# Kernel tuning notes

Measured on AMD Instinct MI355X. Metric: run time of the kernel, lower is better.

Reference implementation:

```python
import jax, jax.numpy as jnp
import numpy as np

B, S, H = 32, 1024, 768          # batch, seq_len, bert hidden
E, W, P = 128, 8, 512            # entities/sample, span width, rel pairs/sample
NT, NR = 5, 9                    # entity types, relation types
D1, HEADS1, D2, RD = 128, 2, 64, 32
REL_IN = 2 * D2 + RD + H         # 928


def _layernorm(x, g, b):
    m = x.mean(-1, keepdims=True)
    v = x.var(-1, keepdims=True)
    return (x - m) * jax.lax.rsqrt(v + 1e-5) * g + b


def _gat_dense(x, Wm, a_src, a_dst, bias, concat):
    # Fully-connected entity graph (incl. self-loops, PyG GATConv default).
    Bn, En, _ = x.shape
    Hh, D = a_src.shape
    h = (x @ Wm).reshape(Bn, En, Hh, D)                      # [B,E,h,D]
    s = jnp.einsum('behd,hd->beh', h, a_src)                 # source score
    d = jnp.einsum('behd,hd->beh', h, a_dst)                 # target score
    # edge j->i : e_ij = leaky_relu(s_j + d_i)
    e = jax.nn.leaky_relu(d[:, :, None, :] + s[:, None, :, :], 0.2)  # [B,i,j,h]
    alpha = jax.nn.softmax(e, axis=2)
    o = jnp.einsum('bijh,bjhd->bihd', alpha, h)
    o = o.reshape(Bn, En, Hh * D) if concat else o.mean(axis=2)
    return o + bias


def setup_inputs() -> dict:
    key = jax.random.key(0)
    ks = jax.random.split(key, 20)
    f = lambda k, shape: jax.random.normal(k, shape, jnp.float32) * 0.02
    return dict(
        sequence_output=jax.random.normal(ks[0], (B, S, H), jnp.float32),
        entity_starts=jax.random.randint(ks[1], (B, E), 0, S - W),
        entity_type_ids=jax.random.randint(ks[2], (B, E), 0, NT),
        pair_idx=jax.random.randint(ks[3], (B, P, 2), 0, E),
        rel_type_ids=jax.random.randint(ks[4], (B, P), 0, NR),
        entity_type_emb=f(ks[5], (NT, H)),
        rel_type_emb=f(ks[6], (NR, RD)),
        W1=f(ks[7], (H, HEADS1 * D1)), a_src1=f(ks[8], (HEADS1, D1)),
        a_dst1=f(ks[9], (HEADS1, D1)), b1=jnp.zeros((HEADS1 * D1,), jnp.float32),
        ln1_g=jnp.ones((HEADS1 * D1,), jnp.float32), ln1_b=jnp.zeros((HEADS1 * D1,), jnp.float32),
        W2=f(ks[10], (HEADS1 * D1, D2)), a_src2=f(ks[11], (1, D2)),
        a_dst2=f(ks[12], (1, D2)), b2=jnp.zeros((D2,), jnp.float32),
        ln2_g=jnp.ones((D2,), jnp.float32), ln2_b=jnp.zeros((D2,), jnp.float32),
        Wr1=f(ks[13], (REL_IN, 256)), br1=jnp.zeros((256,), jnp.float32),
        Wr2=f(ks[14], (256, 1)), br2=jnp.zeros((1,), jnp.float32),
    )


def reference(sequence_output, entity_starts, entity_type_ids, pair_idx, rel_type_ids,
              entity_type_emb, rel_type_emb,
              W1, a_src1, a_dst1, b1, ln1_g, ln1_b,
              W2, a_src2, a_dst2, b2, ln2_g, ln2_b,
              Wr1, br1, Wr2, br2):
    bidx = jnp.arange(B)[:, None]
    # --- per-entity attention pooling over span tokens ---
    tok_idx = entity_starts[:, :, None] + jnp.arange(W)            # [B,E,W]
    toks = sequence_output[jnp.arange(B)[:, None, None], tok_idx]  # [B,E,W,H]
    mean = toks.mean(axis=2)                                       # [B,E,H]
    attn = jax.nn.softmax(jnp.einsum('bewh,beh->bew', toks, mean), axis=-1)
    pooled = jnp.einsum('bew,bewh->beh', attn, toks)
    x = pooled + entity_type_emb[entity_type_ids]                  # [B,E,H]
    # --- 2-layer GAT over fully-connected entity graph ---
    x = jax.nn.elu(_layernorm(_gat_dense(x, W1, a_src1, a_dst1, b1, True), ln1_g, ln1_b))
    x = jax.nn.elu(_layernorm(_gat_dense(x, W2, a_src2, a_dst2, b2, False), ln2_g, ln2_b))
    # --- gather-concat relation MLP scoring ---
    cls = sequence_output[:, 0, :]                                 # [B,H]
    x1 = x[bidx, pair_idx[:, :, 0]]                                # [B,P,64]
    x2 = x[bidx, pair_idx[:, :, 1]]
    rel = rel_type_emb[rel_type_ids]                               # [B,P,32]
    pv = jnp.concatenate([x1, x2, rel, jnp.broadcast_to(cls[:, None, :], (B, P, H))], axis=-1)
    scores = (jax.nn.relu(pv @ Wr1 + br1) @ Wr2 + br2)[..., 0]     # [B,P]
    return scores
```

## Files before the change

### kernel.cpp

```cpp
#include <hip/hip_runtime.h>
#include <hip/hip_bf16.h>

#define BB 32
#define SS 1024
#define HHH 768
#define EE 128
#define WW 8
#define PP 512
#define RDD 32

typedef __attribute__((ext_vector_type(8))) short bf16x8;
typedef __attribute__((ext_vector_type(8))) unsigned short us8;
typedef __attribute__((ext_vector_type(4))) unsigned short us4;
typedef __attribute__((ext_vector_type(4))) float f32x4;

__device__ __forceinline__ unsigned short f2bf(float v) {
    __hip_bfloat16 h = __float2bfloat16(v);
    return *(unsigned short*)&h;
}
__device__ __forceinline__ float bf2f(unsigned short u) {
    unsigned int x = ((unsigned int)u) << 16;
    float f; __builtin_memcpy(&f, &x, 4);
    return f;
}

__global__ __launch_bounds__(256) void pool_prep_kernel(
    const float* __restrict__ seq, const int* __restrict__ starts,
    const int* __restrict__ types, const float* __restrict__ temb,
    unsigned short* __restrict__ xout,
    const float* __restrict__ W1, unsigned short* __restrict__ Wt,
    const float* __restrict__ Wr1, unsigned short* __restrict__ Wtr,
    const float* __restrict__ W2, unsigned short* __restrict__ W2t,
    const float* __restrict__ remb, unsigned short* __restrict__ rembb,
    float* __restrict__ basep) {
    int tid = threadIdx.x;
    __shared__ float sbuf[WW * HHH];
    __shared__ float scred[WW];
    __shared__ float attn_s[WW];

    if (blockIdx.x < BB * EE) {
        int be = blockIdx.x;
        int b = be >> 7;
        int start = starts[be];
        const float4* bp4 = (const float4*)(seq + ((size_t)b * SS + start) * HHH);
        for (int idx = tid; idx < WW * (HHH / 4); idx += 256) {
            int w = idx / (HHH / 4), h4 = idx % (HHH / 4);
            float4 v = bp4[(size_t)w * (HHH / 4) + h4];
            sbuf[w * HHH + h4 * 4 + 0] = v.x; sbuf[w * HHH + h4 * 4 + 1] = v.y;
            sbuf[w * HHH + h4 * 4 + 2] = v.z; sbuf[w * HHH + h4 * 4 + 3] = v.w;
        }
        __syncthreads();

        float sc[WW];
#pragma unroll
        for (int w = 0; w < WW; w++) sc[w] = 0.f;
#pragma unroll
        for (int c = 0; c < 3; c++) {
            int h = tid + 256 * c;
            float s = 0.f;
#pragma unroll
            for (int w = 0; w < WW; w++) s += sbuf[w * HHH + h];
            float m = s * (1.0f / WW);
#pragma unroll
            for (int w = 0; w < WW; w++) sc[w] += sbuf[w * HHH + h] * m;
        }
        if (tid < WW) scred[tid] = 0.f;
        __syncthreads();
        int lane = tid & 63;
#pragma unroll
        for (int w = 0; w < WW; w++) {
            float v = sc[w];
            for (int o = 32; o > 0; o >>= 1) v += __shfl_down(v, o, 64);
            if (lane == 0) atomicAdd(&scred[w], v);
        }
        __syncthreads();
        if (tid == 0) {
            float mx = scred[0];
            for (int w = 1; w < WW; w++) mx = fmaxf(mx, scred[w]);
            float ssum = 0.f;
            float a[WW];
            for (int w = 0; w < WW; w++) { a[w] = __expf(scred[w] - mx); ssum += a[w]; }
            float inv = 1.f / ssum;
            for (int w = 0; w < WW; w++) attn_s[w] = a[w] * inv;
        }
        __syncthreads();

        int t = types[be];
        const float* emb = temb + (size_t)t * HHH;
#pragma unroll
        for (int c = 0; c < 3; c++) {
            int h = tid + 256 * c;
            float p = 0.f;
#pragma unroll
            for (int w = 0; w < WW; w++) p += attn_s[w] * sbuf[w * HHH + h];
            xout[(size_t)be * HHH + h] = f2bf(p + emb[h]);
        }
        return;
    }

    int blk = blockIdx.x - BB * EE;
    if (blk < 48) {
        int k0 = blk * 16;
        for (int i = tid; i < 16 * 256; i += 256)
            sbuf[i] = W1[(size_t)(k0 + (i >> 8)) * 256 + (i & 255)];
        __syncthreads();
        int n = tid;
        us8 v0, v1;
#pragma unroll
        for (int kk = 0; kk < 8; kk++) v0[kk] = f2bf(sbuf[kk * 256 + n]);
#pragma unroll
        for (int kk = 0; kk < 8; kk++) v1[kk] = f2bf(sbuf[(8 + kk) * 256 + n]);
        *(us8*)(Wt + (size_t)n * HHH + k0) = v0;
        *(us8*)(Wt + (size_t)n * HHH + k0 + 8) = v1;
    } else if (blk < 58) {
        int k0 = (blk - 48) * 16;
        for (int i = tid; i < 16 * 256; i += 256)
            sbuf[i] = Wr1[(size_t)(k0 + (i >> 8)) * 256 + (i & 255)];
        __syncthreads();
        int n = tid;
        us8 v0, v1;
#pragma unroll
        for (int kk = 0; kk < 8; kk++) v0[kk] = f2bf(sbuf[kk * 256 + n]);
#pragma unroll
        for (int kk = 0; kk < 8; kk++) v1[kk] = f2bf(sbuf[(8 + kk) * 256 + n]);
        *(us8*)(Wtr + (size_t)n * 160 + k0) = v0;
        *(us8*)(Wtr + (size_t)n * 160 + k0 + 8) = v1;
    } else if (blk < 74) {
        int k0 = (blk - 58) * 16;
        for (int i = tid; i < 16 * 64; i += 256)
            sbuf[(i >> 6) * 64 + (i & 63)] = W2[(size_t)(k0 + (i >> 6)) * 64 + (i & 63)];
        __syncthreads();
        if (tid < 64) {
            int n = tid;
            us8 v0, v1;
#pragma unroll
            for (int kk = 0; kk < 8; kk++) v0[kk] = f2bf(sbuf[kk * 64 + n]);
#pragma unroll
            for (int kk = 0; kk < 8; kk++) v1[kk] = f2bf(sbuf[(8 + kk) * 64 + n]);
            *(us8*)(W2t + (size_t)n * 256 + k0) = v0;
            *(us8*)(W2t + (size_t)n * 256 + k0 + 8) = v1;
        }
    } else if (blk == 74) {
        for (int i = tid; i < 9 * RDD; i += 256) rembb[i] = f2bf(remb[i]);
    } else {
        int pc = blk - 75;
        int kc = pc % 12;
        int b = pc / 12;
        int n = tid;
        if (n < 64) sbuf[4096 + n] = seq[(size_t)b * SS * HHH + kc * 64 + n];
        __syncthreads();
        float acc = 0.f;
        const float* w = Wr1 + (size_t)(160 + kc * 64) * 256 + n;
#pragma unroll 16
        for (int k = 0; k < 64; k++) acc += sbuf[4096 + k] * w[(size_t)k * 256];
        basep[((size_t)kc * 32 + b) * 256 + n] = acc;
    }
}

__global__ __launch_bounds__(256) void gemm1_mfma_kernel(
    const unsigned short* __restrict__ Xb, const unsigned short* __restrict__ Wt,
    float* __restrict__ C) {
    const int K = HHH;
    int n0 = blockIdx.x * 64;
    int m0 = blockIdx.y * 64;
    int tid = threadIdx.x;
    int wave = tid >> 6, lane = tid & 63;
    int wm = (wave >> 1) * 32, wn = (wave & 1) * 32;

    __shared__ __align__(16) unsigned short As[64][40];
    __shared__ __align__(16) unsigned short Bs[64][40];

    f32x4 acc[2][2] = {};
    int ar = tid >> 2;
    int ac = (tid & 3) * 8;
    int fr = lane & 15;
    int fk = (lane >> 4) * 8;

    for (int k0 = 0; k0 < K; k0 += 32) {
        us8 av = *(const us8*)(Xb + (size_t)(m0 + ar) * K + k0 + ac);
        us8 bv = *(const us8*)(Wt + (size_t)(n0 + ar) * K + k0 + ac);
        *(us8*)(&As[ar][ac]) = av;
        *(us8*)(&Bs[ar][ac]) = bv;
        __syncthreads();

        bf16x8 a0 = *(const bf16x8*)(&As[wm + fr][fk]);
        bf16x8 a1 = *(const bf16x8*)(&As[wm + 16 + fr][fk]);
        bf16x8 b0 = *(const bf16x8*)(&Bs[wn + fr][fk]);
        bf16x8 b1 = *(const bf16x8*)(&Bs[wn + 16 + fr][fk]);

        acc[0][0] = __builtin_amdgcn_mfma_f32_16x16x32_bf16(a0, b0, acc[0][0], 0, 0, 0);
        acc[0][1] = __builtin_amdgcn_mfma_f32_16x16x32_bf16(a0, b1, acc[0][1], 0, 0, 0);
        acc[1][0] = __builtin_amdgcn_mfma_f32_16x16x32_bf16(a1, b0, acc[1][0], 0, 0, 0);
        acc[1][1] = __builtin_amdgcn_mfma_f32_16x16x32_bf16(a1, b1, acc[1][1], 0, 0, 0);
        __syncthreads();
    }

    int crow = (lane >> 4) * 4;
    int ccol = lane & 15;
#pragma unroll
    for (int mi = 0; mi < 2; mi++)
#pragma unroll
        for (int ni = 0; ni < 2; ni++)
#pragma unroll
            for (int r = 0; r < 4; r++)
                C[(size_t)(m0 + wm + mi * 16 + crow + r) * 256 +
                  n0 + wn + ni * 16 + ccol] = acc[mi][ni][r];
}

__global__ __launch_bounds__(256) void gat1_fused_kernel(
    const float* __restrict__ h1, const float* __restrict__ a_src1,
    const float* __restrict__ a_dst1, const float* __restrict__ b1,
    const float* __restrict__ gamma, const float* __restrict__ beta,
    unsigned short* __restrict__ g1b) {
    int b = blockIdx.x;
    int tid = threadIdx.x;
    int wave = tid >> 6, lane = tid & 63;
    int wm = wave * 32;
    int fr = lane & 15;
    int fk = (lane >> 4) * 8;

    __shared__ __align__(16) unsigned short h1T[2][128][136];
    __shared__ float ssh[2][128];
    __shared__ float dsh[2][128];

    {
        const float4* src4 = (const float4*)(h1 + (size_t)b * 128 * 256);
        for (int it = 0; it < 32; it++) {
            int i4 = tid + it * 256;
            int j = i4 >> 6;
            int c4 = i4 & 63;
            float4 v = src4[(size_t)j * 64 + c4];
            int d = c4 * 4;
            int hh = d >> 7, dl = d & 127;
            h1T[hh][dl + 0][j] = f2bf(v.x);
            h1T[hh][dl + 1][j] = f2bf(v.y);
            h1T[hh][dl + 2][j] = f2bf(v.z);
            h1T[hh][dl + 3][j] = f2bf(v.w);
        }
    }
    __syncthreads();

    {
        int hh = tid >> 7, j = tid & 127;
        const float* as = a_src1 + hh * 128;
        const float* ad = a_dst1 + hh * 128;
        float s_ = 0.f, d_ = 0.f;
        for (int d2 = 0; d2 < 128; d2++) {
            float hv = bf2f(h1T[hh][d2][j]);
            s_ += hv * as[d2];
            d_ += hv * ad[d2];
        }
        ssh[hh][j] = s_;
        dsh[hh][j] = d_;
    }
    __syncthreads();

    bf16x8 afrag[2][2][4];
#pragma unroll
    for (int hh = 0; hh < 2; hh++)
#pragma unroll
        for (int mi = 0; mi < 2; mi++) {
            int i = wm + mi * 16 + fr;
            float dd = dsh[hh][i];
            float ev[4][8];
            float mx = -1e30f;
#pragma unroll
            for (int ks = 0; ks < 4; ks++)
#pragma unroll
                for (int jj = 0; jj < 8; jj++) {
                    float e = dd + ssh[hh][ks * 32 + fk + jj];
                    e = e >= 0.f ? e : 0.2f * e;
                    ev[ks][jj] = e;
                    mx = fmaxf(mx, e);
                }
            mx = fmaxf(mx, __shfl_xor(mx, 16, 64));
            mx = fmaxf(mx, __shfl_xor(mx, 32, 64));
            float sm = 0.f;
#pragma unroll
            for (int ks = 0; ks < 4; ks++)
#pragma unroll
                for (int jj = 0; jj < 8; jj++) {
                    float e = __expf(ev[ks][jj] - mx);
                    ev[ks][jj] = e;
                    sm += e;
                }
            sm += __shfl_xor(sm, 16, 64);
            sm += __shfl_xor(sm, 32, 64);
            float inv = 1.f / sm;
#pragma unroll
            for (int ks = 0; ks < 4; ks++) {
                bf16x8 a;
#pragma unroll
                for (int jj = 0; jj < 8; jj++)
                    a[jj] = (short)f2bf(ev[ks][jj] * inv);
                afrag[hh][mi][ks] = a;
            }
        }

    f32x4 acc[2][16] = {};
#pragma unroll
    for (int ks = 0; ks < 4; ks++)
#pragma unroll
        for (int ni = 0; ni < 16; ni++) {
            int hh = ni >> 3;
            bf16x8 bv = *(const bf16x8*)(&h1T[hh][(ni & 7) * 16 + fr][ks * 32 + fk]);
            acc[0][ni] = __builtin_amdgcn_mfma_f32_16x16x32_bf16(
                afrag[hh][0][ks], bv, acc[0][ni], 0, 0, 0);
            acc[1][ni] = __builtin_amdgcn_mfma_f32_16x16x32_bf16(
                afrag[hh][1][ks], bv, acc[1][ni], 0, 0, 0);
        }

    int crow = (lane >> 4) * 4;
    int ccol = lane & 15;
    float bv_[16], gv[16], bev[16];
#pragma unroll
    for (int ni = 0; ni < 16; ni++) {
        int d = ni * 16 + ccol;
        bv_[ni] = b1[d]; gv[ni] = gamma[d]; bev[ni] = beta[d];
    }
#pragma unroll
    for (int mi = 0; mi < 2; mi++)
#pragma unroll
        for (int r = 0; r < 4; r++) {
            float v[16];
            float s = 0.f;
#pragma unroll
            for (int ni = 0; ni < 16; ni++) {
                v[ni] = acc[mi][ni][r] + bv_[ni];
                s += v[ni];
            }
            s += __shfl_xor(s, 1, 64); s += __shfl_xor(s, 2, 64);
            s += __shfl_xor(s, 4, 64); s += __shfl_xor(s, 8, 64);
            float mean = s * (1.f / 256.f);
            float sq = 0.f;
#pragma unroll
            for (int ni = 0; ni < 16; ni++) {
                float dv = v[ni] - mean;
                sq += dv * dv;
            }
            sq += __shfl_xor(sq, 1, 64); sq += __shfl_xor(sq, 2, 64);
            sq += __shfl_xor(sq, 4, 64); sq += __shfl_xor(sq, 8, 64);
            float rs = rsqrtf(sq * (1.f / 256.f) + 1e-5f);
            int i = wm + mi * 16 + crow + r;
            unsigned short* dst = g1b + (size_t)(b * 128 + i) * 256;
#pragma unroll
            for (int ni = 0; ni < 16; ni++) {
                float y = (v[ni] - mean) * rs * gv[ni] + bev[ni];
                y = y > 0.f ? y : (__expf(y) - 1.f);
                dst[ni * 16 + ccol] = f2bf(y);
            }
        }
}

__global__ __launch_bounds__(256) void gemm2_mfma_kernel(
    const unsigned short* __restrict__ g1b, const unsigned short* __restrict__ W2t,
    const float* __restrict__ asrc, const float* __restrict__ adst,
    float* __restrict__ h2, float* __restrict__ s2, float* __restrict__ d2) {
    int m0 = blockIdx.x * 64;
    int tid = threadIdx.x;
    int wave = tid >> 6, lane = tid & 63;
    int wm = (wave >> 1) * 32, wn = (wave & 1) * 32;

    __shared__ __align__(16) unsigned short As[64][72];
    __shared__ __align__(16) unsigned short Bs[64][72];
    __shared__ float sdred[64][2][2];

    f32x4 acc[2][2] = {};
    int fr = lane & 15;
    int fk = (lane >> 4) * 8;

    for (int kc = 0; kc < 4; kc++) {
        for (int it = 0; it < 2; it++) {
            int i = tid + it * 256;
            int row = i >> 3, c = i & 7;
            *(us8*)(&As[row][c * 8]) =
                *(const us8*)(g1b + (size_t)(m0 + row) * 256 + kc * 64 + c * 8);
            *(us8*)(&Bs[row][c * 8]) =
                *(const us8*)(W2t + (size_t)row * 256 + kc * 64 + c * 8);
        }
        __syncthreads();
#pragma unroll
        for (int ks = 0; ks < 2; ks++) {
            int kb = ks * 32 + fk;
            bf16x8 a0 = *(const bf16x8*)(&As[wm + fr][kb]);
            bf16x8 a1 = *(const bf16x8*)(&As[wm + 16 + fr][kb]);
            bf16x8 b0 = *(const bf16x8*)(&Bs[wn + fr][kb]);
            bf16x8 b1 = *(const bf16x8*)(&Bs[wn + 16 + fr][kb]);
            acc[0][0] = __builtin_amdgcn_mfma_f32_16x16x32_bf16(a0, b0, acc[0][0], 0, 0, 0);
            acc[0][1] = __builtin_amdgcn_mfma_f32_16x16x32_bf16(a0, b1, acc[0][1], 0, 0, 0);
            acc[1][0] = __builtin_amdgcn_mfma_f32_16x16x32_bf16(a1, b0, acc[1][0], 0, 0, 0);
            acc[1][1] = __builtin_amdgcn_mfma_f32_16x16x32_bf16(a1, b1, acc[1][1], 0, 0, 0);
        }
        __syncthreads();
    }

    int crow = (lane >> 4) * 4;
    int ccol = lane & 15;
    float asv[2], adv[2];
#pragma unroll
    for (int ni = 0; ni < 2; ni++) {
        int n = wn + ni * 16 + ccol;
        asv[ni] = asrc[n];
        adv[ni] = adst[n];
    }
#pragma unroll
    for (int mi = 0; mi < 2; mi++) {
#pragma unroll
        for (int r = 0; r < 4; r++) {
            float sp = 0.f, dp = 0.f;
#pragma unroll
            for (int ni = 0; ni < 2; ni++) {
                float v = acc[mi][ni][r];
                h2[(size_t)(m0 + wm + mi * 16 + crow + r) * 64 +
                   wn + ni * 16 + ccol] = v;
                sp += v * asv[ni];
                dp += v * adv[ni];
            }
            for (int msk = 1; msk < 16; msk <<= 1) {
                sp += __shfl_xor(sp, msk, 64);
                dp += __shfl_xor(dp, msk, 64);
            }
            if ((lane & 15) == 0) {
                int row = wm + mi * 16 + crow + r;
                sdred[row][wn >> 5][0] = sp;
                sdred[row][wn >> 5][1] = dp;
            }
        }
    }
    __syncthreads();
    if (tid < 64 && wave == 0) {
        s2[m0 + tid] = sdred[tid][0][0] + sdred[tid][1][0];
        d2[m0 + tid] = sdred[tid][0][1] + sdred[tid][1][1];
    }
}

__global__ __launch_bounds__(256) void gat2_fused_kernel(
    const float* __restrict__ h2, const float* __restrict__ s2,
    const float* __restrict__ d2, const float* __restrict__ b2v,
    const float* __restrict__ gamma, const float* __restrict__ beta,
    unsigned short* __restrict__ x2b) {
    int b = blockIdx.x;
    int tid = threadIdx.x;
    int wave = tid >> 6, lane = tid & 63;
    int wm = wave * 32;
    int fr = lane & 15;
    int fk = (lane >> 4) * 8;

    __shared__ __align__(16) unsigned short h2T[64][136];
    __shared__ float ssh[128];
    __shared__ float dsh[128];

    {
        const float4* src4 = (const float4*)(h2 + (size_t)b * 128 * 64);
        for (int it = 0; it < 8; it++) {
            int i4 = tid + it * 256;
            int j = i4 >> 4;
            int c4 = i4 & 15;
            float4 v = src4[(size_t)j * 16 + c4];
            int d = c4 * 4;
            h2T[d + 0][j] = f2bf(v.x);
            h2T[d + 1][j] = f2bf(v.y);
            h2T[d + 2][j] = f2bf(v.z);
            h2T[d + 3][j] = f2bf(v.w);
        }
        if (tid < 128) ssh[tid] = s2[(size_t)b * 128 + tid];
        else dsh[tid - 128] = d2[(size_t)b * 128 + (tid - 128)];
    }
    __syncthreads();

    bf16x8 afrag[2][4];
#pragma unroll
    for (int mi = 0; mi < 2; mi++) {
        int i = wm + mi * 16 + fr;
        float dd = dsh[i];
        float ev[4][8];
        float mx = -1e30f;
#pragma unroll
        for (int ks = 0; ks < 4; ks++)
#pragma unroll
            for (int jj = 0; jj < 8; jj++) {
                float e = dd + ssh[ks * 32 + fk + jj];
                e = e >= 0.f ? e : 0.2f * e;
                ev[ks][jj] = e;
                mx = fmaxf(mx, e);
            }
        mx = fmaxf(mx, __shfl_xor(mx, 16, 64));
        mx = fmaxf(mx, __shfl_xor(mx, 32, 64));
        float sm = 0.f;
#pragma unroll
        for (int ks = 0; ks < 4; ks++)
#pragma unroll
            for (int jj = 0; jj < 8; jj++) {
                float e = __expf(ev[ks][jj] - mx);
                ev[ks][jj] = e;
                sm += e;
            }
        sm += __shfl_xor(sm, 16, 64);
        sm += __shfl_xor(sm, 32, 64);
        float inv = 1.f / sm;
#pragma unroll
        for (int ks = 0; ks < 4; ks++) {
            bf16x8 a;
#pragma unroll
            for (int jj = 0; jj < 8; jj++)
                a[jj] = (short)f2bf(ev[ks][jj] * inv);
            afrag[mi][ks] = a;
        }
    }

    f32x4 acc[2][4] = {};
#pragma unroll
    for (int ks = 0; ks < 4; ks++)
#pragma unroll
        for (int ni = 0; ni < 4; ni++) {
            bf16x8 bv = *(const bf16x8*)(&h2T[ni * 16 + fr][ks * 32 + fk]);
            acc[0][ni] = __builtin_amdgcn_mfma_f32_16x16x32_bf16(
                afrag[0][ks], bv, acc[0][ni], 0, 0, 0);
            acc[1][ni] = __builtin_amdgcn_mfma_f32_16x16x32_bf16(
                afrag[1][ks], bv, acc[1][ni], 0, 0, 0);
        }

    int crow = (lane >> 4) * 4;
    int ccol = lane & 15;
    float bv_[4], gv[4], bev[4];
#pragma unroll
    for (int ni = 0; ni < 4; ni++) {
        int d = ni * 16 + ccol;
        bv_[ni] = b2v[d]; gv[ni] = gamma[d]; bev[ni] = beta[d];
    }
#pragma unroll
    for (int mi = 0; mi < 2; mi++)
#pragma unroll
        for (int r = 0; r < 4; r++) {
            float v[4];
            float s = 0.f;
#pragma unroll
            for (int ni = 0; ni < 4; ni++) {
                v[ni] = acc[mi][ni][r] + bv_[ni];
                s += v[ni];
            }
            s += __shfl_xor(s, 1, 64); s += __shfl_xor(s, 2, 64);
            s += __shfl_xor(s, 4, 64); s += __shfl_xor(s, 8, 64);
            float mean = s * (1.f / 64.f);
            float sq = 0.f;
#pragma unroll
            for (int ni = 0; ni < 4; ni++) {
                float dv = v[ni] - mean;
                sq += dv * dv;
            }
            sq += __shfl_xor(sq, 1, 64); sq += __shfl_xor(sq, 2, 64);
            sq += __shfl_xor(sq, 4, 64); sq += __shfl_xor(sq, 8, 64);
            float rs = rsqrtf(sq * (1.f / 64.f) + 1e-5f);
            int i = wm + mi * 16 + crow + r;
            unsigned short* dst = x2b + (size_t)(b * 128 + i) * 64;
#pragma unroll
            for (int ni = 0; ni < 4; ni++) {
                float y = (v[ni] - mean) * rs * gv[ni] + bev[ni];
                y = y > 0.f ? y : (__expf(y) - 1.f);
                dst[ni * 16 + ccol] = f2bf(y);
            }
        }
}

__global__ __launch_bounds__(256) void score_mfma_kernel(
    const unsigned short* __restrict__ x2b, const float* __restrict__ basep,
    const float* __restrict__ br1,
    const int* __restrict__ pair_idx, const int* __restrict__ rel_ids,
    const unsigned short* __restrict__ rembb, const unsigned short* __restrict__ Wtr,
    const float* __restrict__ Wr2, const float* __restrict__ br2,
    float* __restrict__ out) {
    int blk = blockIdx.x;
    int b = blk >> 3;
    int p0 = (blk & 7) * 64;
    int tid = threadIdx.x;
    int wave = tid >> 6, lane = tid & 63;
    int wn = wave * 64;

    __shared__ __align__(16) unsigned short As[64][168];
    __shared__ __align__(16) unsigned short Bs[256][40];
    __shared__ float sred[64][4];
    __shared__ int prs[64][3];

    if (tid < 64) {
        int p = p0 + tid;
        prs[tid][0] = pair_idx[((size_t)b * PP + p) * 2 + 0];
        prs[tid][1] = pair_idx[((size_t)b * PP + p) * 2 + 1];
        prs[tid][2] = rel_ids[(size_t)b * PP + p];
    }
    __syncthreads();
    for (int it = 0; it < 10; it++) {
        int idx = tid + it * 256;
        int m = idx / 40, c = idx % 40;
        int k0 = c * 4;
        us4 v;
        if (k0 < 64)
            v = *(const us4*)(x2b + ((size_t)b * EE + prs[m][0]) * 64 + k0);
        else if (k0 < 128)
            v = *(const us4*)(x2b + ((size_t)b * EE + prs[m][1]) * 64 + (k0 - 64));
        else
            v = *(const us4*)(rembb + prs[m][2] * RDD + (k0 - 128));
        *(us4*)(&As[m][k0]) = v;
    }

    f32x4 acc[4][4] = {};
    int fr = lane & 15;
    int fk = (lane >> 4) * 8;

    for (int kc = 0; kc < 5; kc++) {
        for (int it = 0; it < 4; it++) {
            int i = tid + it * 256;
            int n = i >> 2, c = i & 3;
            *(us8*)(&Bs[n][c * 8]) =
                *(const us8*)(Wtr + (size_t)n * 160 + kc * 32 + c * 8);
        }
        __syncthreads();
        bf16x8 a[4], bv[4];
#pragma unroll
        for (int mi = 0; mi < 4; mi++)
            a[mi] = *(const bf16x8*)(&As[mi * 16 + fr][kc * 32 + fk]);
#pragma unroll
        for (int ni = 0; ni < 4; ni++)
            bv[ni] = *(const bf16x8*)(&Bs[wn + ni * 16 + fr][fk]);
#pragma unroll
        for (int mi = 0; mi < 4; mi++)
#pragma unroll
            for (int ni = 0; ni < 4; ni++)
                acc[mi][ni] = __builtin_amdgcn_mfma_f32_16x16x32_bf16(
                    a[mi], bv[ni], acc[mi][ni], 0, 0, 0);
        __syncthreads();
    }

    int crow = (lane >> 4) * 4;
    int ccol = lane & 15;
    float basev[4], w2v[4];
#pragma unroll
    for (int ni = 0; ni < 4; ni++) {
        int n = wn + ni * 16 + ccol;
        float bb = br1[n];
#pragma unroll
        for (int kc = 0; kc < 12; kc++)
            bb += basep[((size_t)kc * 32 + b) * 256 + n];
        basev[ni] = bb;
        w2v[ni] = Wr2[n];
    }
#pragma unroll
    for (int mi = 0; mi < 4; mi++) {
#pragma unroll
        for (int r = 0; r < 4; r++) {
            float p = 0.f;
#pragma unroll
            for (int ni = 0; ni < 4; ni++)
                p += fmaxf(acc[mi][ni][r] + basev[ni], 0.f) * w2v[ni];
            for (int msk = 1; msk < 16; msk <<= 1)
                p += __shfl_xor(p, msk, 64);
            if ((lane & 15) == 0)
                sred[mi * 16 + crow + r][wave] = p;
        }
    }
    __syncthreads();
    if (tid < 64) {
        float s = sred[tid][0] + sred[tid][1] + sred[tid][2] + sred[tid][3] + br2[0];
        out[(size_t)b * PP + p0 + tid] = s;
    }
}

extern "C" void kernel_launch(void* const* d_in, const int* in_sizes, int n_in,
                              void* d_out, int out_size, void* d_ws, size_t ws_size,
                              hipStream_t stream) {
    (void)in_sizes; (void)n_in; (void)out_size; (void)ws_size;
    const float* seq      = (const float*)d_in[0];
    const int*   starts   = (const int*)d_in[1];
    const int*   types    = (const int*)d_in[2];
    const int*   pair_idx = (const int*)d_in[3];
    const int*   rel_ids  = (const int*)d_in[4];
    const float* temb     = (const float*)d_in[5];
    const float* remb     = (const float*)d_in[6];
    const float* W1       = (const float*)d_in[7];
    const float* a_src1   = (const float*)d_in[8];
    const float* a_dst1   = (const float*)d_in[9];
    const float* b1       = (const float*)d_in[10];
    const float* ln1_g    = (const float*)d_in[11];
    const float* ln1_b    = (const float*)d_in[12];
    const float* W2       = (const float*)d_in[13];
    const float* a_src2   = (const float*)d_in[14];
    const float* a_dst2   = (const float*)d_in[15];
    const float* b2       = (const float*)d_in[16];
    const float* ln2_g    = (const float*)d_in[17];
    const float* ln2_b    = (const float*)d_in[18];
    const float* Wr1      = (const float*)d_in[19];
    const float* br1      = (const float*)d_in[20];
    const float* Wr2      = (const float*)d_in[21];
    const float* br2      = (const float*)d_in[22];
    float* out = (float*)d_out;

    unsigned short* xb    = (unsigned short*)d_ws;
    unsigned short* Wt    = xb + (size_t)4096 * 768;
    unsigned short* Wtr   = Wt + (size_t)256 * 768;
    unsigned short* W2t   = Wtr + (size_t)256 * 160;
    unsigned short* rembb = W2t + (size_t)64 * 256;
    unsigned short* g1b   = rembb + 512;
    unsigned short* x2b   = g1b + (size_t)4096 * 256;
    float* fbase = (float*)(x2b + (size_t)4096 * 64);
    float* h1    = fbase;
    float* h2    = h1 + (size_t)4096 * 256;
    float* s2    = h2 + (size_t)4096 * 64;
    float* d2    = s2 + 4096;
    float* basep = d2 + 4096;

    pool_prep_kernel<<<BB * EE + 75 + 12 * 32, 256, 0, stream>>>(
        seq, starts, types, temb, xb, W1, Wt, Wr1, Wtr, W2, W2t, remb, rembb, basep);
    gemm1_mfma_kernel<<<dim3(4, 64), 256, 0, stream>>>(xb, Wt, h1);
    gat1_fused_kernel<<<BB, 256, 0, stream>>>(h1, a_src1, a_dst1, b1, ln1_g, ln1_b, g1b);
    gemm2_mfma_kernel<<<64, 256, 0, stream>>>(g1b, W2t, a_src2, a_dst2, h2, s2, d2);
    gat2_fused_kernel<<<BB, 256, 0, stream>>>(h2, s2, d2, b2, ln2_g, ln2_b, x2b);
    score_mfma_kernel<<<BB * PP / 64, 256, 0, stream>>>(x2b, basep, br1, pair_idx,
                                                        rel_ids, rembb, Wtr, Wr2,
                                                        br2, out);
}
```

Baseline: 250.9 us.

## Split GAT attention kernels across more blocks and precompute layer-1 scores

The layer-1 GAT kernel now launches 4 blocks per sample, each covering 32 target rows with one head per wave pair. LayerNorm statistics are combined across the two heads through shared memory using a sum and sum-of-squares form. The source and destination attention scores move into a separate small kernel that reduces each row with wave shuffles. Layer 2 is likewise split into 2 blocks per sample. The aim is to fill more compute units than 32 blocks can and to drop the serial per-thread score loop, at the cost of reloading h1 per block, an extra launch, and a slightly less stable variance formula.

```diff
diff --git a/kernel.cpp b/kernel.cpp
--- a/kernel.cpp
+++ b/kernel.cpp
@@ -207,21 +207,41 @@
                   n0 + wn + ni * 16 + ccol] = acc[mi][ni][r];
 }
 
+__global__ void sd1_kernel(const float* __restrict__ h1, const float* __restrict__ asrc,
+                           const float* __restrict__ adst, float* __restrict__ s1,
+                           float* __restrict__ d1) {
+    int beh = blockIdx.x;
+    int h = beh & 1;
+    int be = beh >> 1;
+    int lane = threadIdx.x;
+    const float* row = h1 + (size_t)be * 256 + h * 128;
+    float v0 = row[lane], v1 = row[lane + 64];
+    float ss = v0 * asrc[h * 128 + lane] + v1 * asrc[h * 128 + lane + 64];
+    float dd = v0 * adst[h * 128 + lane] + v1 * adst[h * 128 + lane + 64];
+    for (int o = 32; o > 0; o >>= 1) {
+        ss += __shfl_down(ss, o, 64);
+        dd += __shfl_down(dd, o, 64);
+    }
+    if (lane == 0) { s1[beh] = ss; d1[beh] = dd; }
+}
+
 __global__ __launch_bounds__(256) void gat1_fused_kernel(
-    const float* __restrict__ h1, const float* __restrict__ a_src1,
-    const float* __restrict__ a_dst1, const float* __restrict__ b1,
+    const float* __restrict__ h1, const float* __restrict__ s1,
+    const float* __restrict__ d1, const float* __restrict__ b1,
     const float* __restrict__ gamma, const float* __restrict__ beta,
     unsigned short* __restrict__ g1b) {
-    int b = blockIdx.x;
+    int b = blockIdx.x >> 2;
+    int c = blockIdx.x & 3;
     int tid = threadIdx.x;
     int wave = tid >> 6, lane = tid & 63;
-    int wm = wave * 32;
+    int h = wave >> 1, m = wave & 1;
     int fr = lane & 15;
     int fk = (lane >> 4) * 8;
 
     __shared__ __align__(16) unsigned short h1T[2][128][136];
     __shared__ float ssh[2][128];
     __shared__ float dsh[2][128];
+    __shared__ float lnred[32][2][2];
 
     {
         const float4* src4 = (const float4*)(h1 + (size_t)b * 128 * 256);
@@ -237,119 +257,105 @@
             h1T[hh][dl + 2][j] = f2bf(v.z);
             h1T[hh][dl + 3][j] = f2bf(v.w);
         }
+        int hh = tid >> 7, j = tid & 127;
+        ssh[hh][j] = s1[((size_t)b * 128 + j) * 2 + hh];
+        dsh[hh][j] = d1[((size_t)b * 128 + j) * 2 + hh];
     }
     __syncthreads();
 
+    bf16x8 afrag[4];
     {
-        int hh = tid >> 7, j = tid & 127;
-        const float* as = a_src1 + hh * 128;
-        const float* ad = a_dst1 + hh * 128;
-        float s_ = 0.f, d_ = 0.f;
-        for (int d2 = 0; d2 < 128; d2++) {
-            float hv = bf2f(h1T[hh][d2][j]);
-            s_ += hv * as[d2];
-            d_ += hv * ad[d2];
-        }
-        ssh[hh][j] = s_;
-        dsh[hh][j] = d_;
-    }
-    __syncthreads();
-
-    bf16x8 afrag[2][2][4];
-#pragma unroll
-    for (int hh = 0; hh < 2; hh++)
-#pragma unroll
-        for (int mi = 0; mi < 2; mi++) {
-            int i = wm + mi * 16 + fr;
-            float dd = dsh[hh][i];
-            float ev[4][8];
-            float mx = -1e30f;
-#pragma unroll
-            for (int ks = 0; ks < 4; ks++)
-#pragma unroll
-                for (int jj = 0; jj < 8; jj++) {
-                    float e = dd + ssh[hh][ks * 32 + fk + jj];
-                    e = e >= 0.f ? e : 0.2f * e;
-                    ev[ks][jj] = e;
-                    mx = fmaxf(mx, e);
-                }
-            mx = fmaxf(mx, __shfl_xor(mx, 16, 64));
-            mx = fmaxf(mx, __shfl_xor(mx, 32, 64));
-            float sm = 0.f;
-#pragma unroll
-            for (int ks = 0; ks < 4; ks++)
-#pragma unroll
-                for (int jj = 0; jj < 8; jj++) {
-                    float e = __expf(ev[ks][jj] - mx);
-                    ev[ks][jj] = e;
-                    sm += e;
-                }
-            sm += __shfl_xor(sm, 16, 64);
-            sm += __shfl_xor(sm, 32, 64);
-            float inv = 1.f / sm;
-#pragma unroll
-            for (int ks = 0; ks < 4; ks++) {
-                bf16x8 a;
-#pragma unroll
-                for (int jj = 0; jj < 8; jj++)
-                    a[jj] = (short)f2bf(ev[ks][jj] * inv);
-                afrag[hh][mi][ks] = a;
+        float dd = dsh[h][c * 32 + m * 16 + fr];
+        float ev[4][8];
+        float mx = -1e30f;
+#pragma unroll
+        for (int ks = 0; ks < 4; ks++)
+#pragma unroll
+            for (int jj = 0; jj < 8; jj++) {
+                float e = dd + ssh[h][ks * 32 + fk + jj];
+                e = e >= 0.f ? e : 0.2f * e;
+                ev[ks][jj] = e;
+                mx = fmaxf(mx, e);
             }
-        }
-
-    f32x4 acc[2][16] = {};
+        mx = fmaxf(mx, __shfl_xor(mx, 16, 64));
+        mx = fmaxf(mx, __shfl_xor(mx, 32, 64));
+        float sm = 0.f;
+#pragma unroll
+        for (int ks = 0; ks < 4; ks++)
+#pragma unroll
+            for (int jj = 0; jj < 8; jj++) {
+                float e = __expf(ev[ks][jj] - mx);
+                ev[ks][jj] = e;
+                sm += e;
+            }
+        sm += __shfl_xor(sm, 16, 64);
+        sm += __shfl_xor(sm, 32, 64);
+        float inv = 1.f / sm;
+#pragma unroll
+        for (int ks = 0; ks < 4; ks++) {
+            bf16x8 a;
+#pragma unroll
+            for (int jj = 0; jj < 8; jj++)
+                a[jj] = (short)f2bf(ev[ks][jj] * inv);
+            afrag[ks] = a;
+        }
+    }
+
+    f32x4 acc[8] = {};
 #pragma unroll
     for (int ks = 0; ks < 4; ks++)
 #pragma unroll
-        for (int ni = 0; ni < 16; ni++) {
-            int hh = ni >> 3;
-            bf16x8 bv = *(const bf16x8*)(&h1T[hh][(ni & 7) * 16 + fr][ks * 32 + fk]);
-            acc[0][ni] = __builtin_amdgcn_mfma_f32_16x16x32_bf16(
-                afrag[hh][0][ks], bv, acc[0][ni], 0, 0, 0);
-            acc[1][ni] = __builtin_amdgcn_mfma_f32_16x16x32_bf16(
-                afrag[hh][1][ks], bv, acc[1][ni], 0, 0, 0);
+        for (int ni = 0; ni < 8; ni++) {
+            bf16x8 bv = *(const bf16x8*)(&h1T[h][ni * 16 + fr][ks * 32 + fk]);
+            acc[ni] = __builtin_amdgcn_mfma_f32_16x16x32_bf16(
+                afrag[ks], bv, acc[ni], 0, 0, 0);
         }
 
     int crow = (lane >> 4) * 4;
     int ccol = lane & 15;
-    float bv_[16], gv[16], bev[16];
-#pragma unroll
-    for (int ni = 0; ni < 16; ni++) {
-        int d = ni * 16 + ccol;
+    float bv_[8], gv[8], bev[8];
+#pragma unroll
+    for (int ni = 0; ni < 8; ni++) {
+        int d = h * 128 + ni * 16 + ccol;
         bv_[ni] = b1[d]; gv[ni] = gamma[d]; bev[ni] = beta[d];
     }
-#pragma unroll
-    for (int mi = 0; mi < 2; mi++)
-#pragma unroll
-        for (int r = 0; r < 4; r++) {
-            float v[16];
-            float s = 0.f;
-#pragma unroll
-            for (int ni = 0; ni < 16; ni++) {
-                v[ni] = acc[mi][ni][r] + bv_[ni];
-                s += v[ni];
-            }
-            s += __shfl_xor(s, 1, 64); s += __shfl_xor(s, 2, 64);
-            s += __shfl_xor(s, 4, 64); s += __shfl_xor(s, 8, 64);
-            float mean = s * (1.f / 256.f);
-            float sq = 0.f;
-#pragma unroll
-            for (int ni = 0; ni < 16; ni++) {
-                float dv = v[ni] - mean;
-                sq += dv * dv;
-            }
-            sq += __shfl_xor(sq, 1, 64); sq += __shfl_xor(sq, 2, 64);
-            sq += __shfl_xor(sq, 4, 64); sq += __shfl_xor(sq, 8, 64);
-            float rs = rsqrtf(sq * (1.f / 256.f) + 1e-5f);
-            int i = wm + mi * 16 + crow + r;
-            unsigned short* dst = g1b + (size_t)(b * 128 + i) * 256;
-#pragma unroll
-            for (int ni = 0; ni < 16; ni++) {
-                float y = (v[ni] - mean) * rs * gv[ni] + bev[ni];
-                y = y > 0.f ? y : (__expf(y) - 1.f);
-                dst[ni * 16 + ccol] = f2bf(y);
-            }
-        }
+    float vv[4][8];
+#pragma unroll
+    for (int r = 0; r < 4; r++) {
+        float s = 0.f, q = 0.f;
+#pragma unroll
+        for (int ni = 0; ni < 8; ni++) {
+            float v = acc[ni][r] + bv_[ni];
+            vv[r][ni] = v;
+            s += v;
+            q += v * v;
+        }
+        s += __shfl_xor(s, 1, 64); s += __shfl_xor(s, 2, 64);
+        s += __shfl_xor(s, 4, 64); s += __shfl_xor(s, 8, 64);
+        q += __shfl_xor(q, 1, 64); q += __shfl_xor(q, 2, 64);
+        q += __shfl_xor(q, 4, 64); q += __shfl_xor(q, 8, 64);
+        if ((lane & 15) == 0) {
+            lnred[m * 16 + crow + r][h][0] = s;
+            lnred[m * 16 + crow + r][h][1] = q;
+        }
+    }
+    __syncthreads();
+#pragma unroll
+    for (int r = 0; r < 4; r++) {
+        int row = m * 16 + crow + r;
+        float s = lnred[row][0][0] + lnred[row][1][0];
+        float q = lnred[row][0][1] + lnred[row][1][1];
+        float mean = s * (1.f / 256.f);
+        float var = q * (1.f / 256.f) - mean * mean;
+        float rs = rsqrtf(var + 1e-5f);
+        unsigned short* dst = g1b + (size_t)(b * 128 + c * 32 + row) * 256 + h * 128;
+#pragma unroll
+        for (int ni = 0; ni < 8; ni++) {
+            float y = (vv[r][ni] - mean) * rs * gv[ni] + bev[ni];
+            y = y > 0.f ? y : (__expf(y) - 1.f);
+            dst[ni * 16 + ccol] = f2bf(y);
+        }
+    }
 }
 
 __global__ __launch_bounds__(256) void gemm2_mfma_kernel(
@@ -439,10 +445,10 @@
     const float* __restrict__ d2, const float* __restrict__ b2v,
     const float* __restrict__ gamma, const float* __restrict__ beta,
     unsigned short* __restrict__ x2b) {
-    int b = blockIdx.x;
+    int b = blockIdx.x >> 1;
+    int c = blockIdx.x & 1;
     int tid = threadIdx.x;
     int wave = tid >> 6, lane = tid & 63;
-    int wm = wave * 32;
     int fr = lane & 15;
     int fk = (lane >> 4) * 8;
 
@@ -468,11 +474,9 @@
     }
     __syncthreads();
 
-    bf16x8 afrag[2][4];
-#pragma unroll
-    for (int mi = 0; mi < 2; mi++) {
-        int i = wm + mi * 16 + fr;
-        float dd = dsh[i];
+    bf16x8 afrag[4];
+    {
+        float dd = dsh[c * 64 + wave * 16 + fr];
         float ev[4][8];
         float mx = -1e30f;
 #pragma unroll
@@ -504,20 +508,18 @@
 #pragma unroll
             for (int jj = 0; jj < 8; jj++)
                 a[jj] = (short)f2bf(ev[ks][jj] * inv);
-            afrag[mi][ks] = a;
-        }
-    }
-
-    f32x4 acc[2][4] = {};
+            afrag[ks] = a;
+        }
+    }
+
+    f32x4 acc[4] = {};
 #pragma unroll
     for (int ks = 0; ks < 4; ks++)
 #pragma unroll
         for (int ni = 0; ni < 4; ni++) {
             bf16x8 bv = *(const bf16x8*)(&h2T[ni * 16 + fr][ks * 32 + fk]);
-            acc[0][ni] = __builtin_amdgcn_mfma_f32_16x16x32_bf16(
-                afrag[0][ks], bv, acc[0][ni], 0, 0, 0);
-            acc[1][ni] = __builtin_amdgcn_mfma_f32_16x16x32_bf16(
-                afrag[1][ks], bv, acc[1][ni], 0, 0, 0);
+            acc[ni] = __builtin_amdgcn_mfma_f32_16x16x32_bf16(
+                afrag[ks], bv, acc[ni], 0, 0, 0);
         }
 
     int crow = (lane >> 4) * 4;
@@ -529,37 +531,35 @@
         bv_[ni] = b2v[d]; gv[ni] = gamma[d]; bev[ni] = beta[d];
     }
 #pragma unroll
-    for (int mi = 0; mi < 2; mi++)
-#pragma unroll
-        for (int r = 0; r < 4; r++) {
-            float v[4];
-            float s = 0.f;
-#pragma unroll
-            for (int ni = 0; ni < 4; ni++) {
-                v[ni] = acc[mi][ni][r] + bv_[ni];
-                s += v[ni];
-            }
-            s += __shfl_xor(s, 1, 64); s += __shfl_xor(s, 2, 64);
-            s += __shfl_xor(s, 4, 64); s += __shfl_xor(s, 8, 64);
-            float mean = s * (1.f / 64.f);
-            float sq = 0.f;
-#pragma unroll
-            for (int ni = 0; ni < 4; ni++) {
-                float dv = v[ni] - mean;
-                sq += dv * dv;
-            }
-            sq += __shfl_xor(sq, 1, 64); sq += __shfl_xor(sq, 2, 64);
-            sq += __shfl_xor(sq, 4, 64); sq += __shfl_xor(sq, 8, 64);
-            float rs = rsqrtf(sq * (1.f / 64.f) + 1e-5f);
-            int i = wm + mi * 16 + crow + r;
-            unsigned short* dst = x2b + (size_t)(b * 128 + i) * 64;
-#pragma unroll
-            for (int ni = 0; ni < 4; ni++) {
-                float y = (v[ni] - mean) * rs * gv[ni] + bev[ni];
-                y = y > 0.f ? y : (__expf(y) - 1.f);
-                dst[ni * 16 + ccol] = f2bf(y);
-            }
-        }
+    for (int r = 0; r < 4; r++) {
+        float v[4];
+        float s = 0.f;
+#pragma unroll
+        for (int ni = 0; ni < 4; ni++) {
+            v[ni] = acc[ni][r] + bv_[ni];
+            s += v[ni];
+        }
+        s += __shfl_xor(s, 1, 64); s += __shfl_xor(s, 2, 64);
+        s += __shfl_xor(s, 4, 64); s += __shfl_xor(s, 8, 64);
+        float mean = s * (1.f / 64.f);
+        float sq = 0.f;
+#pragma unroll
+        for (int ni = 0; ni < 4; ni++) {
+            float dv = v[ni] - mean;
+            sq += dv * dv;
+        }
+        sq += __shfl_xor(sq, 1, 64); sq += __shfl_xor(sq, 2, 64);
+        sq += __shfl_xor(sq, 4, 64); sq += __shfl_xor(sq, 8, 64);
+        float rs = rsqrtf(sq * (1.f / 64.f) + 1e-5f);
+        int i = c * 64 + wave * 16 + crow + r;
+        unsigned short* dst = x2b + (size_t)(b * 128 + i) * 64;
+#pragma unroll
+        for (int ni = 0; ni < 4; ni++) {
+            float y = (v[ni] - mean) * rs * gv[ni] + bev[ni];
+            y = y > 0.f ? y : (__expf(y) - 1.f);
+            dst[ni * 16 + ccol] = f2bf(y);
+        }
+    }
 }
 
 __global__ __launch_bounds__(256) void score_mfma_kernel(
@@ -702,7 +702,9 @@
     unsigned short* x2b   = g1b + (size_t)4096 * 256;
     float* fbase = (float*)(x2b + (size_t)4096 * 64);
     float* h1    = fbase;
-    float* h2    = h1 + (size_t)4096 * 256;
+    float* s1    = h1 + (size_t)4096 * 256;
+    float* d1    = s1 + 8192;
+    float* h2    = d1 + 8192;
     float* s2    = h2 + (size_t)4096 * 64;
     float* d2    = s2 + 4096;
     float* basep = d2 + 4096;
@@ -710,9 +712,10 @@
     pool_prep_kernel<<<BB * EE + 75 + 12 * 32, 256, 0, stream>>>(
         seq, starts, types, temb, xb, W1, Wt, Wr1, Wtr, W2, W2t, remb, rembb, basep);
     gemm1_mfma_kernel<<<dim3(4, 64), 256, 0, stream>>>(xb, Wt, h1);
-    gat1_fused_kernel<<<BB, 256, 0, stream>>>(h1, a_src1, a_dst1, b1, ln1_g, ln1_b, g1b);
+    sd1_kernel<<<BB * EE * 2, 64, 0, stream>>>(h1, a_src1, a_dst1, s1, d1);
+    gat1_fused_kernel<<<BB * 4, 256, 0, stream>>>(h1, s1, d1, b1, ln1_g, ln1_b, g1b);
     gemm2_mfma_kernel<<<64, 256, 0, stream>>>(g1b, W2t, a_src2, a_dst2, h2, s2, d2);
-    gat2_fused_kernel<<<BB, 256, 0, stream>>>(h2, s2, d2, b2, ln2_g, ln2_b, x2b);
+    gat2_fused_kernel<<<BB * 2, 256, 0, stream>>>(h2, s2, d2, b2, ln2_g, ln2_b, x2b);
     score_mfma_kernel<<<BB * PP / 64, 256, 0, stream>>>(x2b, basep, br1, pair_idx,
                                                         rel_ids, rembb, Wtr, Wr2,
                                                         br2, out);
```

Measured after the change: 242.3 us. -3.4%, faster.
